# Kernel optimization log

Hardware: AMD Instinct MI355X
Metric: run time of the kernel (lower is better)

## Reference

```python
import jax, jax.numpy as jnp
import numpy as np

N, E = 50000, 800000
DIM_IN, DIM_H, DIM_OUT, HEADS = 128, 16, 64, 8
NEG_SLOPE = 0.2  # PyG GATv2Conv default


def setup_inputs() -> dict:
    key = jax.random.key(0)
    ks = jax.random.split(key, 10)
    s = 0.1
    x = jax.random.normal(ks[0], (N, DIM_IN), jnp.float32)
    edge_index = jax.random.randint(ks[1], (2, E), 0, N, dtype=jnp.int32)
    Wl1 = jax.random.normal(ks[2], (DIM_IN, HEADS * DIM_H), jnp.float32) * s
    Wr1 = jax.random.normal(ks[3], (DIM_IN, HEADS * DIM_H), jnp.float32) * s
    att1 = jax.random.normal(ks[4], (HEADS, DIM_H), jnp.float32) * s
    b1 = jnp.zeros((HEADS * DIM_H,), jnp.float32)
    Wl2 = jax.random.normal(ks[5], (HEADS * DIM_H, DIM_OUT), jnp.float32) * s
    Wr2 = jax.random.normal(ks[6], (HEADS * DIM_H, DIM_OUT), jnp.float32) * s
    att2 = jax.random.normal(ks[7], (1, DIM_OUT), jnp.float32) * s
    b2 = jnp.zeros((DIM_OUT,), jnp.float32)
    return dict(x=x, edge_index=edge_index, Wl1=Wl1, Wr1=Wr1, att1=att1, b1=b1,
                Wl2=Wl2, Wr2=Wr2, att2=att2, b2=b2)


def gatv2_conv(x, src, dst, Wl, Wr, att, bias, heads, out_ch):
    # PyG GATv2Conv (share_weights=False, concat=True)
    n = x.shape[0]
    xl = (x @ Wl).reshape(n, heads, out_ch)  # source-side transform
    xr = (x @ Wr).reshape(n, heads, out_ch)  # target-side transform
    e = jax.nn.leaky_relu(xl[src] + xr[dst], NEG_SLOPE)          # [E, H, C]
    logits = jnp.einsum('ehc,hc->eh', e, att)                    # [E, H]
    # segment softmax over incoming edges of each dst node
    m = jax.lax.stop_gradient(jax.ops.segment_max(logits, dst, num_segments=n))
    ex = jnp.exp(logits - m[dst])
    denom = jax.ops.segment_sum(ex, dst, num_segments=n)
    alpha = ex / denom[dst]                                      # [E, H]
    out = jax.ops.segment_sum(xl[src] * alpha[..., None], dst, num_segments=n)
    return out.reshape(n, heads * out_ch) + bias


def reference(x, edge_index, Wl1, Wr1, att1, b1, Wl2, Wr2, att2, b2):
    n = x.shape[0]
    loops = jnp.arange(n, dtype=edge_index.dtype)
    src = jnp.concatenate([edge_index[0], loops])  # add_self_loops=True
    dst = jnp.concatenate([edge_index[1], loops])
    h = gatv2_conv(x, src, dst, Wl1, Wr1, att1, b1, HEADS, DIM_H)
    h = jax.nn.elu(h)
    out = gatv2_conv(h, src, dst, Wl2, Wr2, att2, b2, 1, DIM_OUT)
    return jax.nn.log_softmax(out, axis=1)
```

## Files before the change

kernel.cpp:

```cpp
#include <hip/hip_runtime.h>
#include <cstdint>

#define DIM_IN 128
#define HEADS 8
#define DIM_H 16
#define H1 128
#define DIM_OUT 64
#define NEG 0.2f
#define CAP 6144

typedef __attribute__((ext_vector_type(8))) short bf16x8;
typedef __attribute__((ext_vector_type(4))) float f32x4;

__device__ __forceinline__ float blo(uint32_t u) { return __uint_as_float(u << 16); }
__device__ __forceinline__ float bhi(uint32_t u) { return __uint_as_float(u & 0xffff0000u); }
__device__ __forceinline__ unsigned short f2b(float f) {
  uint32_t u = __float_as_uint(f);
  u += 0x7fffu + ((u >> 16) & 1u);
  return (unsigned short)(u >> 16);
}

#define KP 0.86561702453337804f
#define KM 0.57707801635558536f

__global__ __launch_bounds__(256) void prep_fused(
    const float* __restrict__ x, unsigned short* __restrict__ xb, int totx,
    const float* __restrict__ W0, const float* __restrict__ W1,
    const float* __restrict__ W2, const float* __restrict__ W3,
    unsigned short* __restrict__ T0, unsigned short* __restrict__ T1,
    unsigned short* __restrict__ T2, unsigned short* __restrict__ T3,
    int xblocks) {
  int bx = blockIdx.x;
  if (bx < xblocks) {
    int i = (bx * 256 + threadIdx.x) * 8;
    if (i >= totx) return;
    float4 a = *(const float4*)(x + i);
    float4 b = *(const float4*)(x + i + 4);
    ushort4 u0 = {f2b(a.x), f2b(a.y), f2b(a.z), f2b(a.w)};
    ushort4 u1 = {f2b(b.x), f2b(b.y), f2b(b.z), f2b(b.w)};
    *(ushort4*)(xb + i) = u0;
    *(ushort4*)(xb + i + 4) = u1;
  } else {
    int wz = bx - xblocks;
    int z = wz >> 6;
    const float* W = (z == 0) ? W0 : (z == 1) ? W1 : (z == 2) ? W2 : W3;
    unsigned short* T = (z == 0) ? T0 : (z == 1) ? T1 : (z == 2) ? T2 : T3;
    int M = (z < 2) ? 128 : 64;
    int t = (wz & 63) * 256 + threadIdx.x;
    if (t >= M * 128) return;
    int n = t >> 7, k = t & 127;
    T[t] = f2b(W[k * M + n]);
  }
}

template <int M>
__global__ __launch_bounds__(256) void gemm_mfma(
    const unsigned short* __restrict__ A,
    const unsigned short* __restrict__ Bt0, const unsigned short* __restrict__ Bt1,
    unsigned short* __restrict__ C0, unsigned short* __restrict__ C1, int Nrows) {
  constexpr int K = 128;
  constexpr int LDA = 72;
  constexpr int MT = M / 2;
  constexpr int NT = MT / 16;
  __shared__ __align__(16) short Asm[128 * LDA];
  __shared__ __align__(16) short Bsm[M * LDA];
  const unsigned short* __restrict__ Bt = blockIdx.z ? Bt1 : Bt0;
  unsigned short* __restrict__ Cb = blockIdx.z ? C1 : C0;
  const int row0 = blockIdx.x * 128;
  const int tid = threadIdx.x;
  const int w = tid >> 6, lane = tid & 63;
  const int l = lane & 15, q = lane >> 4;
  const int wrow = (w >> 1) * 64, wcol = (w & 1) * MT;

  f32x4 zero = {0.f, 0.f, 0.f, 0.f};
  f32x4 acc[4][NT];
#pragma unroll
  for (int ti = 0; ti < 4; ++ti)
#pragma unroll
    for (int tj = 0; tj < NT; ++tj) acc[ti][tj] = zero;

  for (int k0 = 0; k0 < K; k0 += 64) {
    __syncthreads();
    {
      int r = tid >> 1, sg = (tid & 1) * 32;
      int grow = row0 + r;
      const uint4* src = (const uint4*)(A + (size_t)grow * K + k0 + sg);
      uint4 z4 = make_uint4(0, 0, 0, 0);
#pragma unroll
      for (int i = 0; i < 4; ++i) {
        uint4 v = (grow < Nrows) ? src[i] : z4;
        *(uint4*)(Asm + r * LDA + sg + i * 8) = v;
      }
    }
    {
      int r = tid >> 1, sg = (tid & 1) * 32;
      if (r < M) {
        const uint4* src = (const uint4*)(Bt + (size_t)r * K + k0 + sg);
#pragma unroll
        for (int i = 0; i < 4; ++i)
          *(uint4*)(Bsm + r * LDA + sg + i * 8) = src[i];
      }
    }
    __syncthreads();
#pragma unroll
    for (int kk = 0; kk < 64; kk += 32) {
      bf16x8 af[4], bfr[NT];
#pragma unroll
      for (int ti = 0; ti < 4; ++ti)
        af[ti] = *(const bf16x8*)(Asm + (wrow + ti * 16 + l) * LDA + kk + q * 8);
#pragma unroll
      for (int tj = 0; tj < NT; ++tj)
        bfr[tj] = *(const bf16x8*)(Bsm + (wcol + tj * 16 + l) * LDA + kk + q * 8);
#pragma unroll
      for (int ti = 0; ti < 4; ++ti)
#pragma unroll
        for (int tj = 0; tj < NT; ++tj)
          acc[ti][tj] = __builtin_amdgcn_mfma_f32_16x16x32_bf16(
              af[ti], bfr[tj], acc[ti][tj], 0, 0, 0);
    }
  }
#pragma unroll
  for (int ti = 0; ti < 4; ++ti) {
#pragma unroll
    for (int tj = 0; tj < NT; ++tj) {
      int col = wcol + tj * 16 + l;
#pragma unroll
      for (int r = 0; r < 4; ++r) {
        int grow = row0 + wrow + ti * 16 + q * 4 + r;
        if (grow < Nrows) Cb[(size_t)grow * M + col] = f2b(acc[ti][tj][r]);
      }
    }
  }
}

__global__ __launch_bounds__(256) void p1_bucket(
    const int* __restrict__ ei, int* __restrict__ gcnt,
    uint32_t* __restrict__ gbuf, int E, int nbkt) {
  __shared__ int hist[256];
  __shared__ int base[256];
  __shared__ int cur[256];
  int tid = threadIdx.x;
  hist[tid] = 0;
  __syncthreads();
  int e0 = blockIdx.x * 8192;
  int nE = min(8192, E - e0);
  for (int i = tid; i < nE; i += 256)
    atomicAdd(&hist[ei[E + e0 + i] >> 8], 1);
  __syncthreads();
  if (tid < nbkt) {
    int h = hist[tid];
    base[tid] = h ? atomicAdd(&gcnt[tid], h) : 0;
  }
  cur[tid] = 0;
  __syncthreads();
  for (int i = tid; i < nE; i += 256) {
    int d = ei[E + e0 + i];
    int s = ei[e0 + i];
    int b = d >> 8;
    int r = atomicAdd(&cur[b], 1);
    int pos = base[b] + r;
    if (pos < CAP) gbuf[(size_t)b * CAP + pos] = ((uint32_t)d << 16) | (uint32_t)s;
  }
}

__device__ __forceinline__ int block_excl_scan256(int v, int* tmp) {
  int lane = threadIdx.x & 63, wid = threadIdx.x >> 6;
  int x = v;
#pragma unroll
  for (int o = 1; o < 64; o <<= 1) {
    int y = __shfl_up(x, o, 64);
    if (lane >= o) x += y;
  }
  if (lane == 63) tmp[wid] = x;
  __syncthreads();
  int prefix = 0;
#pragma unroll
  for (int w = 0; w < 4; ++w) if (w < wid) prefix += tmp[w];
  __syncthreads();
  return prefix + x - v;
}

__global__ __launch_bounds__(256) void p2_fused(
    const uint32_t* __restrict__ gbuf, const int* __restrict__ gcnt,
    int* __restrict__ off, int* __restrict__ srcs, int N, int nbkt) {
  __shared__ int sb[256];
  __shared__ int hist[256];
  __shared__ int cur[256];
  __shared__ int tmp[4];
  int b = blockIdx.x, tid = threadIdx.x;
  int gv = (tid < nbkt) ? gcnt[tid] : 0;
  int gex = block_excl_scan256(gv, tmp);
  sb[tid] = gex;
  hist[tid] = 0;
  __syncthreads();
  int base = sb[b];
  int cnt = min(gcnt[b], CAP);
  const uint32_t* p = gbuf + (size_t)b * CAP;
  for (int i = tid; i < cnt; i += 256)
    atomicAdd(&hist[(p[i] >> 16) & 255], 1);
  __syncthreads();
  int d = hist[tid];
  int excl = block_excl_scan256(d, tmp);
  int idx = (b << 8) + tid;
  int o = base + excl;
  if (idx <= N) off[idx] = o;
  cur[tid] = o;
  __syncthreads();
  for (int i = tid; i < cnt; i += 256) {
    uint32_t v = p[i];
    int pos = atomicAdd(&cur[(v >> 16) & 255], 1);
    srcs[pos] = (int)(v & 0xFFFFu);
  }
}

__global__ __launch_bounds__(256) void agg_l1(
    const int* __restrict__ srcs, const int* __restrict__ off,
    const unsigned short* __restrict__ xlb, const unsigned short* __restrict__ xrb,
    const float* __restrict__ att, const float* __restrict__ b1,
    unsigned short* __restrict__ hbb, int N) {
  int wid = threadIdx.x >> 6, lane = threadIdx.x & 63;
  int node = blockIdx.x * 4 + wid;
  if (node >= N) return;
  const int l4 = lane & 15;
  const int g  = lane >> 4;
  uint4 xru = *(const uint4*)(xrb + ((size_t)node << 7) + (l4 << 3));
  float r0 = blo(xru.x), r1 = bhi(xru.x), r2 = blo(xru.y), r3 = bhi(xru.y);
  float r4 = blo(xru.z), r5 = bhi(xru.z), r6 = blo(xru.w), r7 = bhi(xru.w);
  float4 a0  = *(const float4*)(att + (l4 << 3));
  float4 a1  = *(const float4*)(att + (l4 << 3) + 4);
  float c0 = KP * a0.x, c1 = KP * a0.y, c2 = KP * a0.z, c3 = KP * a0.w;
  float c4 = KP * a1.x, c5 = KP * a1.y, c6 = KP * a1.z, c7 = KP * a1.w;
  float d0 = KM * a0.x, d1 = KM * a0.y, d2 = KM * a0.z, d3 = KM * a0.w;
  float d4 = KM * a1.x, d5 = KM * a1.y, d6 = KM * a1.z, d7 = KM * a1.w;
  float acc0 = 0.f, acc1 = 0.f, acc2 = 0.f, acc3 = 0.f;
  float acc4 = 0.f, acc5 = 0.f, acc6 = 0.f, acc7 = 0.f;
  float dsum = 0.f;
  const uint32_t lo4 = (uint32_t)(l4 << 4);
  int beg = off[node];
  int M = off[node + 1] - beg + 1;
  for (int base = 0; base < M; base += 64) {
    int nk = min(64, M - base);
    int v = base + lane;
    int sv = 0;
    if (lane < nk) sv = (v == 0) ? node : srcs[beg + v - 1];
    int niter = (nk + 3) >> 2;
    int s0 = __shfl(sv, g, 64);
    uint4 xu = *(const uint4*)((const char*)xlb + (((uint32_t)s0 << 8) | lo4));
    for (int it = 0; it < niter; ++it) {
      int j = (it << 2) + g;
      uint4 xc = xu;
      if (it + 1 < niter) {
        int sn = __shfl(sv, j + 4, 64);
        xu = *(const uint4*)((const char*)xlb + (((uint32_t)sn << 8) | lo4));
      }
      float x0 = blo(xc.x), x1 = bhi(xc.x), x2 = blo(xc.y), x3 = bhi(xc.y);
      float x4 = blo(xc.z), x5 = bhi(xc.z), x6 = blo(xc.w), x7 = bhi(xc.w);
      float t, pa, pb;
      t = x0 + r0; pa = c0 * t;          pb = d0 * fabsf(t);
      t = x1 + r1; pa = fmaf(c1, t, pa); pb = fmaf(d1, fabsf(t), pb);
      t = x2 + r2; pa = fmaf(c2, t, pa); pb = fmaf(d2, fabsf(t), pb);
      t = x3 + r3; pa = fmaf(c3, t, pa); pb = fmaf(d3, fabsf(t), pb);
      t = x4 + r4; pa = fmaf(c4, t, pa); pb = fmaf(d4, fabsf(t), pb);
      t = x5 + r5; pa = fmaf(c5, t, pa); pb = fmaf(d5, fabsf(t), pb);
      t = x6 + r6; pa = fmaf(c6, t, pa); pb = fmaf(d6, fabsf(t), pb);
      t = x7 + r7; pa = fmaf(c7, t, pa); pb = fmaf(d7, fabsf(t), pb);
      float p = pa + pb;
      p += __shfl_xor(p, 1, 64);
      float ev = (j < nk) ? __builtin_amdgcn_exp2f(p) : 0.f;
      acc0 = fmaf(ev, x0, acc0); acc1 = fmaf(ev, x1, acc1);
      acc2 = fmaf(ev, x2, acc2); acc3 = fmaf(ev, x3, acc3);
      acc4 = fmaf(ev, x4, acc4); acc5 = fmaf(ev, x5, acc5);
      acc6 = fmaf(ev, x6, acc6); acc7 = fmaf(ev, x7, acc7);
      dsum += ev;
    }
  }
#pragma unroll
  for (int o = 16; o <= 32; o <<= 1) {
    dsum += __shfl_xor(dsum, o, 64);
    acc0 += __shfl_xor(acc0, o, 64); acc1 += __shfl_xor(acc1, o, 64);
    acc2 += __shfl_xor(acc2, o, 64); acc3 += __shfl_xor(acc3, o, 64);
    acc4 += __shfl_xor(acc4, o, 64); acc5 += __shfl_xor(acc5, o, 64);
    acc6 += __shfl_xor(acc6, o, 64); acc7 += __shfl_xor(acc7, o, 64);
  }
  if (g == 0) {
    float inv = 1.0f / dsum;
    float4 bv0 = *(const float4*)(b1 + (l4 << 3));
    float4 bv1 = *(const float4*)(b1 + (l4 << 3) + 4);
    float o0 = fmaf(acc0, inv, bv0.x), o1 = fmaf(acc1, inv, bv0.y);
    float o2 = fmaf(acc2, inv, bv0.z), o3 = fmaf(acc3, inv, bv0.w);
    float o4 = fmaf(acc4, inv, bv1.x), o5 = fmaf(acc5, inv, bv1.y);
    float o6 = fmaf(acc6, inv, bv1.z), o7 = fmaf(acc7, inv, bv1.w);
    o0 = o0 > 0.f ? o0 : expm1f(o0); o1 = o1 > 0.f ? o1 : expm1f(o1);
    o2 = o2 > 0.f ? o2 : expm1f(o2); o3 = o3 > 0.f ? o3 : expm1f(o3);
    o4 = o4 > 0.f ? o4 : expm1f(o4); o5 = o5 > 0.f ? o5 : expm1f(o5);
    o6 = o6 > 0.f ? o6 : expm1f(o6); o7 = o7 > 0.f ? o7 : expm1f(o7);
    ushort4 h0 = {f2b(o0), f2b(o1), f2b(o2), f2b(o3)};
    ushort4 h1 = {f2b(o4), f2b(o5), f2b(o6), f2b(o7)};
    unsigned short* ph = hbb + ((size_t)node << 7) + (l4 << 3);
    *(ushort4*)(ph)     = h0;
    *(ushort4*)(ph + 4) = h1;
  }
}

__global__ __launch_bounds__(256) void agg_l2(
    const int* __restrict__ srcs, const int* __restrict__ off,
    const unsigned short* __restrict__ xlb, const unsigned short* __restrict__ xrb,
    const float* __restrict__ att, const float* __restrict__ b2,
    float* __restrict__ out, int N) {
  int wid = threadIdx.x >> 6, lane = threadIdx.x & 63;
  int node = blockIdx.x * 4 + wid;
  if (node >= N) return;
  const int l3 = lane & 7;
  const int g  = lane >> 3;
  uint4 xru = *(const uint4*)(xrb + ((size_t)node << 6) + (l3 << 3));
  float r0 = blo(xru.x), r1 = bhi(xru.x), r2 = blo(xru.y), r3 = bhi(xru.y);
  float r4 = blo(xru.z), r5 = bhi(xru.z), r6 = blo(xru.w), r7 = bhi(xru.w);
  float4 a0  = *(const float4*)(att + (l3 << 3));
  float4 a1  = *(const float4*)(att + (l3 << 3) + 4);
  float c0 = KP * a0.x, c1 = KP * a0.y, c2 = KP * a0.z, c3 = KP * a0.w;
  float c4 = KP * a1.x, c5 = KP * a1.y, c6 = KP * a1.z, c7 = KP * a1.w;
  float d0 = KM * a0.x, d1 = KM * a0.y, d2 = KM * a0.z, d3 = KM * a0.w;
  float d4 = KM * a1.x, d5 = KM * a1.y, d6 = KM * a1.z, d7 = KM * a1.w;
  float acc0 = 0.f, acc1 = 0.f, acc2 = 0.f, acc3 = 0.f;
  float acc4 = 0.f, acc5 = 0.f, acc6 = 0.f, acc7 = 0.f;
  float dsum = 0.f;
  const uint32_t lo3 = (uint32_t)(l3 << 4);
  int beg = off[node];
  int M = off[node + 1] - beg + 1;
  for (int base = 0; base < M; base += 64) {
    int nk = min(64, M - base);
    int v = base + lane;
    int sv = 0;
    if (lane < nk) sv = (v == 0) ? node : srcs[beg + v - 1];
    int niter = (nk + 7) >> 3;
    int s0 = __shfl(sv, g, 64);
    uint4 xu = *(const uint4*)((const char*)xlb + (((uint32_t)s0 << 7) | lo3));
    for (int it = 0; it < niter; ++it) {
      int j = (it << 3) + g;
      uint4 xc = xu;
      if (it + 1 < niter) {
        int sn = __shfl(sv, j + 8, 64);
        xu = *(const uint4*)((const char*)xlb + (((uint32_t)sn << 7) | lo3));
      }
      float x0 = blo(xc.x), x1 = bhi(xc.x), x2 = blo(xc.y), x3 = bhi(xc.y);
      float x4 = blo(xc.z), x5 = bhi(xc.z), x6 = blo(xc.w), x7 = bhi(xc.w);
      float t, pa, pb;
      t = x0 + r0; pa = c0 * t;          pb = d0 * fabsf(t);
      t = x1 + r1; pa = fmaf(c1, t, pa); pb = fmaf(d1, fabsf(t), pb);
      t = x2 + r2; pa = fmaf(c2, t, pa); pb = fmaf(d2, fabsf(t), pb);
      t = x3 + r3; pa = fmaf(c3, t, pa); pb = fmaf(d3, fabsf(t), pb);
      t = x4 + r4; pa = fmaf(c4, t, pa); pb = fmaf(d4, fabsf(t), pb);
      t = x5 + r5; pa = fmaf(c5, t, pa); pb = fmaf(d5, fabsf(t), pb);
      t = x6 + r6; pa = fmaf(c6, t, pa); pb = fmaf(d6, fabsf(t), pb);
      t = x7 + r7; pa = fmaf(c7, t, pa); pb = fmaf(d7, fabsf(t), pb);
      float p = pa + pb;
      p += __shfl_xor(p, 1, 64);
      p += __shfl_xor(p, 2, 64);
      p += __shfl_xor(p, 4, 64);
      float ev = (j < nk) ? __builtin_amdgcn_exp2f(p) : 0.f;
      acc0 = fmaf(ev, x0, acc0); acc1 = fmaf(ev, x1, acc1);
      acc2 = fmaf(ev, x2, acc2); acc3 = fmaf(ev, x3, acc3);
      acc4 = fmaf(ev, x4, acc4); acc5 = fmaf(ev, x5, acc5);
      acc6 = fmaf(ev, x6, acc6); acc7 = fmaf(ev, x7, acc7);
      dsum += ev;
    }
  }
#pragma unroll
  for (int o = 8; o <= 32; o <<= 1) {
    dsum += __shfl_xor(dsum, o, 64);
    acc0 += __shfl_xor(acc0, o, 64); acc1 += __shfl_xor(acc1, o, 64);
    acc2 += __shfl_xor(acc2, o, 64); acc3 += __shfl_xor(acc3, o, 64);
    acc4 += __shfl_xor(acc4, o, 64); acc5 += __shfl_xor(acc5, o, 64);
    acc6 += __shfl_xor(acc6, o, 64); acc7 += __shfl_xor(acc7, o, 64);
  }
  float inv = 1.0f / dsum;
  float4 bv0 = *(const float4*)(b2 + (l3 << 3));
  float4 bv1 = *(const float4*)(b2 + (l3 << 3) + 4);
  float v0 = fmaf(acc0, inv, bv0.x), v1 = fmaf(acc1, inv, bv0.y);
  float v2 = fmaf(acc2, inv, bv0.z), v3 = fmaf(acc3, inv, bv0.w);
  float v4 = fmaf(acc4, inv, bv1.x), v5 = fmaf(acc5, inv, bv1.y);
  float v6 = fmaf(acc6, inv, bv1.z), v7 = fmaf(acc7, inv, bv1.w);
  float m = fmaxf(fmaxf(fmaxf(v0, v1), fmaxf(v2, v3)),
                  fmaxf(fmaxf(v4, v5), fmaxf(v6, v7)));
#pragma unroll
  for (int o = 1; o <= 4; o <<= 1) m = fmaxf(m, __shfl_xor(m, o, 64));
  float s = __expf(v0 - m) + __expf(v1 - m) + __expf(v2 - m) + __expf(v3 - m)
          + __expf(v4 - m) + __expf(v5 - m) + __expf(v6 - m) + __expf(v7 - m);
#pragma unroll
  for (int o = 1; o <= 4; o <<= 1) s += __shfl_xor(s, o, 64);
  if (g == 0) {
    float ls = __logf(s) + m;
    float* po = out + ((size_t)node << 6) + (l3 << 3);
    *(float4*)(po)     = make_float4(v0 - ls, v1 - ls, v2 - ls, v3 - ls);
    *(float4*)(po + 4) = make_float4(v4 - ls, v5 - ls, v6 - ls, v7 - ls);
  }
}

extern "C" void kernel_launch(void* const* d_in, const int* in_sizes, int n_in,
                              void* d_out, int out_size, void* d_ws, size_t ws_size,
                              hipStream_t stream) {
  const float* x    = (const float*)d_in[0];
  const int*   ei   = (const int*)d_in[1];
  const float* Wl1  = (const float*)d_in[2];
  const float* Wr1  = (const float*)d_in[3];
  const float* att1 = (const float*)d_in[4];
  const float* b1   = (const float*)d_in[5];
  const float* Wl2  = (const float*)d_in[6];
  const float* Wr2  = (const float*)d_in[7];
  const float* att2 = (const float*)d_in[8];
  const float* b2   = (const float*)d_in[9];
  float* out = (float*)d_out;

  const int N = in_sizes[0] / DIM_IN;
  const int E = in_sizes[1] / 2;
  const int nb = (N + 255) / 256;

  unsigned short* us = (unsigned short*)d_ws;
  const size_t szNH = (size_t)N * H1;
  unsigned short* xb   = us;
  unsigned short* xlb1 = xb + szNH;
  unsigned short* xrb1 = xlb1 + szNH;
  unsigned short* hbb  = xrb1 + szNH;
  unsigned short* xlb2 = hbb + szNH;
  unsigned short* xrb2 = xlb2 + (size_t)N * DIM_OUT;
  unsigned short* wt0  = xrb2 + (size_t)N * DIM_OUT;
  unsigned short* wt1  = wt0 + 16384;
  unsigned short* wt2  = wt1 + 16384;
  unsigned short* wt3  = wt2 + 8192;
  int* ibase  = (int*)(wt3 + 8192);
  int* off    = ibase;
  int* gcnt   = ibase + N + 1;
  int* srcs   = ibase + N + 1 + 256;
  uint32_t* gbuf = (uint32_t*)(srcs + E);

  hipMemsetAsync(gcnt, 0, 256 * sizeof(int), stream);
  p1_bucket<<<(E + 8191) / 8192, 256, 0, stream>>>(ei, gcnt, gbuf, E, nb);
  p2_fused<<<nb, 256, 0, stream>>>(gbuf, gcnt, off, srcs, N, nb);

  int totx = N * DIM_IN;
  int xblocks = (totx / 8 + 255) / 256;
  prep_fused<<<xblocks + 256, 256, 0, stream>>>(
      x, xb, totx, Wl1, Wr1, Wl2, Wr2, wt0, wt1, wt2, wt3, xblocks);

  const int gb = (N + 127) / 128;

  gemm_mfma<128><<<dim3(gb, 1, 2), 256, 0, stream>>>(xb, wt0, wt1, xlb1, xrb1, N);
  agg_l1<<<(N + 3) / 4, 256, 0, stream>>>(srcs, off, xlb1, xrb1, att1, b1, hbb, N);

  gemm_mfma<64><<<dim3(gb, 1, 2), 256, 0, stream>>>(hbb, wt2, wt3, xlb2, xrb2, N);
  agg_l2<<<(N + 3) / 4, 256, 0, stream>>>(srcs, off, xlb2, xrb2, att2, b2, out, N);
}
```

Measured before the change: 258.2 us.

## Fuse CSR bucketing passes into prep and layer-1 GEMM launches

Runs the edge bucketing pass as extra blocks of the conversion kernel, and the per-bucket CSR build as extra blocks of the first GEMM launch. The goal is to cut two kernel launches and let the independent graph-preprocessing work overlap with the dense work. The agg kernels also drop their software-prefetch of the next gathered row and load each row directly, which shortens the loop but loses memory-latency hiding. This relies on the bucketing blocks in the merged launch finishing before the CSR blocks read gcnt, which kernel ordering on the stream guarantees.

Result: faster. 247.5 us (-4.1%).

```diff
diff --git a/kernel.cpp b/kernel.cpp
--- a/kernel.cpp
+++ b/kernel.cpp
@@ -23,13 +23,16 @@
 #define KP 0.86561702453337804f
 #define KM 0.57707801635558536f
 
-__global__ __launch_bounds__(256) void prep_fused(
+__global__ __launch_bounds__(256) void prep_p1_fused(
     const float* __restrict__ x, unsigned short* __restrict__ xb, int totx,
     const float* __restrict__ W0, const float* __restrict__ W1,
     const float* __restrict__ W2, const float* __restrict__ W3,
     unsigned short* __restrict__ T0, unsigned short* __restrict__ T1,
     unsigned short* __restrict__ T2, unsigned short* __restrict__ T3,
-    int xblocks) {
+    int xblocks,
+    const int* __restrict__ ei, int* __restrict__ gcnt,
+    uint32_t* __restrict__ gbuf, int E, int nbkt) {
+  __shared__ int sh[768];
   int bx = blockIdx.x;
   if (bx < xblocks) {
     int i = (bx * 256 + threadIdx.x) * 8;
@@ -40,7 +43,7 @@
     ushort4 u1 = {f2b(b.x), f2b(b.y), f2b(b.z), f2b(b.w)};
     *(ushort4*)(xb + i) = u0;
     *(ushort4*)(xb + i + 4) = u1;
-  } else {
+  } else if (bx < xblocks + 256) {
     int wz = bx - xblocks;
     int z = wz >> 6;
     const float* W = (z == 0) ? W0 : (z == 1) ? W1 : (z == 2) ? W2 : W3;
@@ -50,20 +53,98 @@
     if (t >= M * 128) return;
     int n = t >> 7, k = t & 127;
     T[t] = f2b(W[k * M + n]);
-  }
+  } else {
+    int* hist = sh;
+    int* base = sh + 256;
+    int* cur  = sh + 512;
+    int tid = threadIdx.x;
+    hist[tid] = 0;
+    __syncthreads();
+    int e0 = (bx - xblocks - 256) * 8192;
+    int nE = min(8192, E - e0);
+    for (int i = tid; i < nE; i += 256)
+      atomicAdd(&hist[ei[E + e0 + i] >> 8], 1);
+    __syncthreads();
+    if (tid < nbkt) {
+      int h = hist[tid];
+      base[tid] = h ? atomicAdd(&gcnt[tid], h) : 0;
+    }
+    cur[tid] = 0;
+    __syncthreads();
+    for (int i = tid; i < nE; i += 256) {
+      int d = ei[E + e0 + i];
+      int s = ei[e0 + i];
+      int b = d >> 8;
+      int r = atomicAdd(&cur[b], 1);
+      int pos = base[b] + r;
+      if (pos < CAP) gbuf[(size_t)b * CAP + pos] = ((uint32_t)d << 16) | (uint32_t)s;
+    }
+  }
+}
+
+__device__ __forceinline__ int block_excl_scan256(int v, int* tmp) {
+  int lane = threadIdx.x & 63, wid = threadIdx.x >> 6;
+  int x = v;
+#pragma unroll
+  for (int o = 1; o < 64; o <<= 1) {
+    int y = __shfl_up(x, o, 64);
+    if (lane >= o) x += y;
+  }
+  if (lane == 63) tmp[wid] = x;
+  __syncthreads();
+  int prefix = 0;
+#pragma unroll
+  for (int w = 0; w < 4; ++w) if (w < wid) prefix += tmp[w];
+  __syncthreads();
+  return prefix + x - v;
 }
 
 template <int M>
 __global__ __launch_bounds__(256) void gemm_mfma(
     const unsigned short* __restrict__ A,
     const unsigned short* __restrict__ Bt0, const unsigned short* __restrict__ Bt1,
-    unsigned short* __restrict__ C0, unsigned short* __restrict__ C1, int Nrows) {
+    unsigned short* __restrict__ C0, unsigned short* __restrict__ C1, int Nrows,
+    int gbx,
+    const uint32_t* __restrict__ gbuf, const int* __restrict__ gcnt,
+    int* __restrict__ off, int* __restrict__ srcs, int Np, int nbkt) {
   constexpr int K = 128;
   constexpr int LDA = 72;
   constexpr int MT = M / 2;
   constexpr int NT = MT / 16;
   __shared__ __align__(16) short Asm[128 * LDA];
   __shared__ __align__(16) short Bsm[M * LDA];
+  if (blockIdx.x >= gbx) {
+    if (blockIdx.z != 0) return;
+    int* sb   = (int*)Asm;
+    int* hist = sb + 256;
+    int* cur  = hist + 256;
+    int* tmp  = cur + 256;
+    int b = blockIdx.x - gbx, tid = threadIdx.x;
+    int gv = (tid < nbkt) ? gcnt[tid] : 0;
+    int gex = block_excl_scan256(gv, tmp);
+    sb[tid] = gex;
+    hist[tid] = 0;
+    __syncthreads();
+    int base = sb[b];
+    int cnt = min(gcnt[b], CAP);
+    const uint32_t* p = gbuf + (size_t)b * CAP;
+    for (int i = tid; i < cnt; i += 256)
+      atomicAdd(&hist[(p[i] >> 16) & 255], 1);
+    __syncthreads();
+    int d = hist[tid];
+    int excl = block_excl_scan256(d, tmp);
+    int idx = (b << 8) + tid;
+    int o = base + excl;
+    if (idx <= Np) off[idx] = o;
+    cur[tid] = o;
+    __syncthreads();
+    for (int i = tid; i < cnt; i += 256) {
+      uint32_t v = p[i];
+      int pos = atomicAdd(&cur[(v >> 16) & 255], 1);
+      srcs[pos] = (int)(v & 0xFFFFu);
+    }
+    return;
+  }
   const unsigned short* __restrict__ Bt = blockIdx.z ? Bt1 : Bt0;
   unsigned short* __restrict__ Cb = blockIdx.z ? C1 : C0;
   const int row0 = blockIdx.x * 128;
@@ -130,86 +211,6 @@
         if (grow < Nrows) Cb[(size_t)grow * M + col] = f2b(acc[ti][tj][r]);
       }
     }
-  }
-}
-
-__global__ __launch_bounds__(256) void p1_bucket(
-    const int* __restrict__ ei, int* __restrict__ gcnt,
-    uint32_t* __restrict__ gbuf, int E, int nbkt) {
-  __shared__ int hist[256];
-  __shared__ int base[256];
-  __shared__ int cur[256];
-  int tid = threadIdx.x;
-  hist[tid] = 0;
-  __syncthreads();
-  int e0 = blockIdx.x * 8192;
-  int nE = min(8192, E - e0);
-  for (int i = tid; i < nE; i += 256)
-    atomicAdd(&hist[ei[E + e0 + i] >> 8], 1);
-  __syncthreads();
-  if (tid < nbkt) {
-    int h = hist[tid];
-    base[tid] = h ? atomicAdd(&gcnt[tid], h) : 0;
-  }
-  cur[tid] = 0;
-  __syncthreads();
-  for (int i = tid; i < nE; i += 256) {
-    int d = ei[E + e0 + i];
-    int s = ei[e0 + i];
-    int b = d >> 8;
-    int r = atomicAdd(&cur[b], 1);
-    int pos = base[b] + r;
-    if (pos < CAP) gbuf[(size_t)b * CAP + pos] = ((uint32_t)d << 16) | (uint32_t)s;
-  }
-}
-
-__device__ __forceinline__ int block_excl_scan256(int v, int* tmp) {
-  int lane = threadIdx.x & 63, wid = threadIdx.x >> 6;
-  int x = v;
-#pragma unroll
-  for (int o = 1; o < 64; o <<= 1) {
-    int y = __shfl_up(x, o, 64);
-    if (lane >= o) x += y;
-  }
-  if (lane == 63) tmp[wid] = x;
-  __syncthreads();
-  int prefix = 0;
-#pragma unroll
-  for (int w = 0; w < 4; ++w) if (w < wid) prefix += tmp[w];
-  __syncthreads();
-  return prefix + x - v;
-}
-
-__global__ __launch_bounds__(256) void p2_fused(
-    const uint32_t* __restrict__ gbuf, const int* __restrict__ gcnt,
-    int* __restrict__ off, int* __restrict__ srcs, int N, int nbkt) {
-  __shared__ int sb[256];
-  __shared__ int hist[256];
-  __shared__ int cur[256];
-  __shared__ int tmp[4];
-  int b = blockIdx.x, tid = threadIdx.x;
-  int gv = (tid < nbkt) ? gcnt[tid] : 0;
-  int gex = block_excl_scan256(gv, tmp);
-  sb[tid] = gex;
-  hist[tid] = 0;
-  __syncthreads();
-  int base = sb[b];
-  int cnt = min(gcnt[b], CAP);
-  const uint32_t* p = gbuf + (size_t)b * CAP;
-  for (int i = tid; i < cnt; i += 256)
-    atomicAdd(&hist[(p[i] >> 16) & 255], 1);
-  __syncthreads();
-  int d = hist[tid];
-  int excl = block_excl_scan256(d, tmp);
-  int idx = (b << 8) + tid;
-  int o = base + excl;
-  if (idx <= N) off[idx] = o;
-  cur[tid] = o;
-  __syncthreads();
-  for (int i = tid; i < cnt; i += 256) {
-    uint32_t v = p[i];
-    int pos = atomicAdd(&cur[(v >> 16) & 255], 1);
-    srcs[pos] = (int)(v & 0xFFFFu);
   }
 }
 
@@ -235,7 +236,6 @@
   float acc0 = 0.f, acc1 = 0.f, acc2 = 0.f, acc3 = 0.f;
   float acc4 = 0.f, acc5 = 0.f, acc6 = 0.f, acc7 = 0.f;
   float dsum = 0.f;
-  const uint32_t lo4 = (uint32_t)(l4 << 4);
   int beg = off[node];
   int M = off[node + 1] - beg + 1;
   for (int base = 0; base < M; base += 64) {
@@ -244,17 +244,12 @@
     int sv = 0;
     if (lane < nk) sv = (v == 0) ? node : srcs[beg + v - 1];
     int niter = (nk + 3) >> 2;
-    int s0 = __shfl(sv, g, 64);
-    uint4 xu = *(const uint4*)((const char*)xlb + (((uint32_t)s0 << 8) | lo4));
     for (int it = 0; it < niter; ++it) {
       int j = (it << 2) + g;
-      uint4 xc = xu;
-      if (it + 1 < niter) {
-        int sn = __shfl(sv, j + 4, 64);
-        xu = *(const uint4*)((const char*)xlb + (((uint32_t)sn << 8) | lo4));
-      }
-      float x0 = blo(xc.x), x1 = bhi(xc.x), x2 = blo(xc.y), x3 = bhi(xc.y);
-      float x4 = blo(xc.z), x5 = bhi(xc.z), x6 = blo(xc.w), x7 = bhi(xc.w);
+      int s = __shfl(sv, j, 64);
+      uint4 xu = *(const uint4*)(xlb + ((size_t)s << 7) + (l4 << 3));
+      float x0 = blo(xu.x), x1 = bhi(xu.x), x2 = blo(xu.y), x3 = bhi(xu.y);
+      float x4 = blo(xu.z), x5 = bhi(xu.z), x6 = blo(xu.w), x7 = bhi(xu.w);
       float t, pa, pb;
       t = x0 + r0; pa = c0 * t;          pb = d0 * fabsf(t);
       t = x1 + r1; pa = fmaf(c1, t, pa); pb = fmaf(d1, fabsf(t), pb);
@@ -324,7 +319,6 @@
   float acc0 = 0.f, acc1 = 0.f, acc2 = 0.f, acc3 = 0.f;
   float acc4 = 0.f, acc5 = 0.f, acc6 = 0.f, acc7 = 0.f;
   float dsum = 0.f;
-  const uint32_t lo3 = (uint32_t)(l3 << 4);
   int beg = off[node];
   int M = off[node + 1] - beg + 1;
   for (int base = 0; base < M; base += 64) {
@@ -333,17 +327,12 @@
     int sv = 0;
     if (lane < nk) sv = (v == 0) ? node : srcs[beg + v - 1];
     int niter = (nk + 7) >> 3;
-    int s0 = __shfl(sv, g, 64);
-    uint4 xu = *(const uint4*)((const char*)xlb + (((uint32_t)s0 << 7) | lo3));
     for (int it = 0; it < niter; ++it) {
       int j = (it << 3) + g;
-      uint4 xc = xu;
-      if (it + 1 < niter) {
-        int sn = __shfl(sv, j + 8, 64);
-        xu = *(const uint4*)((const char*)xlb + (((uint32_t)sn << 7) | lo3));
-      }
-      float x0 = blo(xc.x), x1 = bhi(xc.x), x2 = blo(xc.y), x3 = bhi(xc.y);
-      float x4 = blo(xc.z), x5 = bhi(xc.z), x6 = blo(xc.w), x7 = bhi(xc.w);
+      int s = __shfl(sv, j, 64);
+      uint4 xu = *(const uint4*)(xlb + ((size_t)s << 6) + (l3 << 3));
+      float x0 = blo(xu.x), x1 = bhi(xu.x), x2 = blo(xu.y), x3 = bhi(xu.y);
+      float x4 = blo(xu.z), x5 = bhi(xu.z), x6 = blo(xu.w), x7 = bhi(xu.w);
       float t, pa, pb;
       t = x0 + r0; pa = c0 * t;          pb = d0 * fabsf(t);
       t = x1 + r1; pa = fmaf(c1, t, pa); pb = fmaf(d1, fabsf(t), pb);
@@ -433,20 +422,24 @@
   int* srcs   = ibase + N + 1 + 256;
   uint32_t* gbuf = (uint32_t*)(srcs + E);
 
+  const int totx = N * DIM_IN;
+  const int xblocks = (totx / 8 + 255) / 256;
+  const int p1b = (E + 8191) / 8192;
+  const int gb = (N + 127) / 128;
+
   hipMemsetAsync(gcnt, 0, 256 * sizeof(int), stream);
-  p1_bucket<<<(E + 8191) / 8192, 256, 0, stream>>>(ei, gcnt, gbuf, E, nb);
-  p2_fused<<<nb, 256, 0, stream>>>(gbuf, gcnt, off, srcs, N, nb);
-
-  int totx = N * DIM_IN;
-  int xblocks = (totx / 8 + 255) / 256;
-  prep_fused<<<xblocks + 256, 256, 0, stream>>>(
-      x, xb, totx, Wl1, Wr1, Wl2, Wr2, wt0, wt1, wt2, wt3, xblocks);
-
-  const int gb = (N + 127) / 128;
-
-  gemm_mfma<128><<<dim3(gb, 1, 2), 256, 0, stream>>>(xb, wt0, wt1, xlb1, xrb1, N);
+
+  prep_p1_fused<<<xblocks + 256 + p1b, 256, 0, stream>>>(
+      x, xb, totx, Wl1, Wr1, Wl2, Wr2, wt0, wt1, wt2, wt3, xblocks,
+      ei, gcnt, gbuf, E, nb);
+
+  gemm_mfma<128><<<dim3(gb + nb, 1, 2), 256, 0, stream>>>(
+      xb, wt0, wt1, xlb1, xrb1, N, gb, gbuf, gcnt, off, srcs, N, nb);
+
   agg_l1<<<(N + 3) / 4, 256, 0, stream>>>(srcs, off, xlb1, xrb1, att1, b1, hbb, N);
 
-  gemm_mfma<64><<<dim3(gb, 1, 2), 256, 0, stream>>>(hbb, wt2, wt3, xlb2, xrb2, N);
+  gemm_mfma<64><<<dim3(gb, 1, 2), 256, 0, stream>>>(
+      hbb, wt2, wt3, xlb2, xrb2, N, gb, nullptr, nullptr, nullptr, nullptr, N, nb);
+
   agg_l2<<<(N + 3) / 4, 256, 0, stream>>>(srcs, off, xlb2, xrb2, att2, b2, out, N);
 }
```
